# Kernel tuning notes

Measured on AMD Instinct MI355X. Metric: run time of the kernel, lower is better.

The kernel has to match this reference:

```python
import jax, jax.numpy as jnp
import numpy as np

D = 256       # vec_dim
HEADS = 8     # head_num
PS = 4        # patch_size
WS = 7        # window_size (in patches)
P = WS * WS   # tokens per window


def _relative_index():
    # replicates the torch meshgrid / relative coord logic (indexing='ij')
    coords = np.stack(np.meshgrid(np.arange(WS), np.arange(WS), indexing='ij'))  # [2,WS,WS]
    cf = coords.reshape(2, -1)                                                   # [2,P]
    rc = (cf[:, :, None] - cf[:, None, :]).transpose(1, 2, 0)                    # [P,P,2]
    rc[:, :, 0] += WS - 1
    rc[:, :, 1] += WS - 1
    rc[:, :, 1] *= 2 * WS - 1
    return rc.sum(-1)  # [P,P] ints in [0,(2WS-1)^2)


def _shift_mask(ch, cw):
    # standard swin shift mask built on the patch grid (ch, cw)
    fm = np.zeros((ch, cw))
    idx = (slice(0, -WS), slice(-WS, -(WS // 2)), slice(-(WS // 2), None))
    cnt = 0
    for y in idx:
        for x in idx:
            fm[y, x] = cnt
            cnt += 1
    nh, nw = ch // WS, cw // WS
    fm = fm.reshape(nh, WS, nw, WS).transpose(0, 2, 1, 3).reshape(nh * nw, P)
    m = fm[:, None, :] - fm[:, :, None]
    return np.where(m != 0, -100.0, 0.0).astype(np.float32)


def setup_inputs() -> dict:
    key = jax.random.key(0)
    ks = jax.random.split(key, 10)
    N, PN = 8, 3136
    s = 0.02
    return {
        'inputs': jax.random.normal(ks[0], (N, D, PN), jnp.float32),
        'Wk': jax.random.normal(ks[1], (HEADS * D, D), jnp.float32) * s,
        'bk': jax.random.normal(ks[2], (HEADS * D,), jnp.float32) * s,
        'Wq': jax.random.normal(ks[3], (HEADS * D, D), jnp.float32) * s,
        'bq': jax.random.normal(ks[4], (HEADS * D,), jnp.float32) * s,
        'Wv': jax.random.normal(ks[5], (HEADS * D, D), jnp.float32) * s,
        'bv': jax.random.normal(ks[6], (HEADS * D,), jnp.float32) * s,
        'Wo': jax.random.normal(ks[7], (D, HEADS * D), jnp.float32) * s,
        'bo': jax.random.normal(ks[8], (D,), jnp.float32) * s,
        'rel_code': jax.random.normal(ks[9], ((2 * WS - 1) ** 2, HEADS), jnp.float32) * 0.02,
        'h': 224,
        'w': 224,
    }


def _forward(inputs, Wk, bk, Wq, bq, Wv, bv, Wo, bo, rel_code, h, w):
    ch, cw = h // PS, w // PS            # patch grid
    N, _, PN = inputs.shape
    C = D // (PS * PS)
    nh, nw = ch // WS, cw // WS
    WIN = nh * nw

    # patches2features -> pixel-space roll by WS//2 -> features2patches
    x = inputs.reshape(N, C, PS, PS, ch, cw)
    x = x.transpose(0, 1, 4, 2, 5, 3).reshape(N, C, ch * PS, cw * PS)
    x = jnp.roll(x, (WS // 2, WS // 2), axis=(-2, -1))
    x = x.reshape(N, C, ch, PS, cw, PS).transpose(0, 2, 4, 1, 3, 5).reshape(N, PN, D)
    x = x.transpose(0, 2, 1)  # [N,D,PN]

    def proj(W, b):
        e = jnp.einsum('od,ndp->nop', W, x) + b[None, :, None]  # [N,HEADS*D,PN]
        e = e.reshape(N, HEADS, D, ch, cw)
        # window partition: n h d (nh w1)(nw w2) -> n h (nh nw) d (w1 w2)
        e = e.reshape(N, HEADS, D, nh, WS, nw, WS)
        return e.transpose(0, 1, 3, 5, 2, 4, 6).reshape(N, HEADS, WIN, D, P)

    k = proj(Wk, bk)
    q = proj(Wq, bq)
    v = proj(Wv, bv)

    # attn[p,q] = k_p . q_q  (softmax over keys p, axis=3)
    attn = jnp.einsum('nhgdp,nhgdq->nhgpq', k, q) / (D ** 0.5)
    mask = jnp.asarray(_shift_mask(ch, cw))
    attn = attn + mask[None, None]
    rel_idx = _relative_index().ravel()
    rel = rel_code[rel_idx].reshape(P, P, HEADS).transpose(2, 0, 1)  # [H,P,P]
    attn = attn + rel[None, :, None]
    wmap = jax.nn.softmax(attn, axis=3)

    out = jnp.einsum('nhgdp,nhgpq->nhgdq', v, wmap)
    # window merge back to [N,H,D,PN]
    out = out.reshape(N, HEADS, nh, nw, D, WS, WS)
    out = out.transpose(0, 1, 4, 2, 5, 3, 6).reshape(N, HEADS * D, PN)
    return jnp.einsum('od,ndp->nop', Wo, out) + bo[None, :, None]  # [N,D,PN]


def reference(inputs, Wk, bk, Wq, bq, Wv, bv, Wo, bo, rel_code, h, w):
    return _forward(inputs, Wk, bk, Wq, bq, Wv, bv, Wo, bo, rel_code, h, w)
```

## Files before the change

### kernel.cpp

```cpp
#include <hip/hip_runtime.h>
#include <hip/hip_bf16.h>


#define NBATCH 8
#define MSTR   2176
#define TROWS  3200

typedef unsigned short ushort_t;
typedef __attribute__((ext_vector_type(8))) short bf16x8;
typedef __attribute__((ext_vector_type(8))) unsigned short u16x8;
typedef __attribute__((ext_vector_type(4))) float f32x4;

__device__ __forceinline__ float b2f(ushort_t u) {
  union { unsigned int i; float f; } v; v.i = ((unsigned int)u) << 16; return v.f;
}
__device__ __forceinline__ ushort_t f2b(float f) {
  union { float f; unsigned int u; } v; v.f = f;
  unsigned int u = v.u;
  return (ushort_t)((u + 0x7FFFu + ((u >> 16) & 1u)) >> 16);
}
__device__ __forceinline__ int regof(int y) { return (y < 49) ? 0 : ((y < 53) ? 1 : 2); }
__device__ __forceinline__ int div7(int t) { return (t * 37) >> 8; }
__device__ __forceinline__ int tmap(int p, int gi, int gj) {
  int wi = div7(p); return (gi * 7 + wi) * 56 + gj * 7 + (p - wi * 7);
}
__device__ __forceinline__ ushort4 pack4(f32x4 a) {
  ushort4 u; u.x = f2b(a[0]); u.y = f2b(a[1]); u.z = f2b(a[2]); u.w = f2b(a[3]);
  return u;
}
__device__ __forceinline__ void gload_lds16(const ushort_t* g, ushort_t* l) {
  __builtin_amdgcn_global_load_lds(
      (const __attribute__((address_space(1))) void*)g,
      (__attribute__((address_space(3))) void*)l, 16, 0, 0);
}

__global__ void k_prep(const float* __restrict__ Wk, const float* __restrict__ Wq,
                       const float* __restrict__ Wo, const float* __restrict__ Wv,
                       const float* __restrict__ bk, const float* __restrict__ bq,
                       const float* __restrict__ bv, const float* __restrict__ bo,
                       const float* __restrict__ relc,
                       ushort_t* __restrict__ Aext, ushort_t* __restrict__ Wov3,
                       float* __restrict__ cvec, float* __restrict__ relL2) {
  __shared__ float red[8];
  int blk = blockIdx.x, t = threadIdx.x;
  if (blk < 512) {
    int h = blk >> 6, b0 = (blk & 63) << 2, a = t;
    const float* wkh = Wk + h * 65536;
    const float* wqh = Wq + h * 65536;
    float a0 = 0.f, a1 = 0.f, a2 = 0.f, a3 = 0.f;
    for (int dd = 0; dd < 256; ++dd) {
      float wk = wkh[dd * 256 + a];
      float4 w4 = *(const float4*)(wqh + dd * 256 + b0);
      a0 += wk * w4.x; a1 += wk * w4.y; a2 += wk * w4.z; a3 += wk * w4.w;
    }
    ushort4 u; u.x = f2b(a0); u.y = f2b(a1); u.z = f2b(a2); u.w = f2b(a3);
    *(ushort4*)(Aext + (h * 256 + a) * 256 + b0) = u;
  } else if (blk < 1024) {
    int bb = blk - 512;
    int h = bb >> 6, o0 = (bb & 63) << 2, d = t;
    float a0 = 0.f, a1 = 0.f, a2 = 0.f, a3 = 0.f;
    for (int dd = 0; dd < 256; ++dd) {
      float wv = Wv[(h * 256 + dd) * 256 + d];
      a0 += Wo[(o0 + 0) * 2048 + h * 256 + dd] * wv;
      a1 += Wo[(o0 + 1) * 2048 + h * 256 + dd] * wv;
      a2 += Wo[(o0 + 2) * 2048 + h * 256 + dd] * wv;
      a3 += Wo[(o0 + 3) * 2048 + h * 256 + dd] * wv;
    }
    Wov3[(o0 + 0) * 2048 + h * 256 + d] = f2b(a0);
    Wov3[(o0 + 1) * 2048 + h * 256 + d] = f2b(a1);
    Wov3[(o0 + 2) * 2048 + h * 256 + d] = f2b(a2);
    Wov3[(o0 + 3) * 2048 + h * 256 + d] = f2b(a3);
  } else if (blk < 1032) {
    int h = blk - 1024;
    float s1 = 0.f, s2 = 0.f;
    for (int dd = 0; dd < 256; ++dd) {
      s1 += bk[h * 256 + dd] * Wq[(h * 256 + dd) * 256 + t];
      s2 += bq[h * 256 + dd] * Wk[(h * 256 + dd) * 256 + t];
    }
    Aext[(2048 + h) * 256 + t] = f2b(s1);
    Aext[(2056 + h) * 256 + t] = f2b(s2);
  } else if (blk == 1032) {
    for (int i = t; i < 112 * 256 / 8; i += 256)
      *(u16x8*)(Aext + 2064 * 256 + i * 8) = (u16x8){0,0,0,0,0,0,0,0};
  } else if (blk < 1289) {
    int o = blk - 1033;
    const float* wob = Wo + o * 2048;
    float acc = 0.f;
#pragma unroll
    for (int j = 0; j < 8; ++j) acc += wob[j * 256 + t] * bv[j * 256 + t];
#pragma unroll
    for (int s = 1; s < 64; s <<= 1) acc += __shfl_xor(acc, s);
    if ((t & 63) == 0) red[t >> 6] = acc;
    __syncthreads();
    if (t == 0) cvec[o] = bo[o] + red[0] + red[1] + red[2] + red[3];
  } else {
    if (t < 8) {
      float c = 0.f;
      for (int dd = 0; dd < 256; ++dd) c += bk[t * 256 + dd] * bq[t * 256 + dd];
      red[t] = c * 0.0625f;
    }
    __syncthreads();
    for (int i = t; i < 8 * 169; i += 256) {
      int h = i / 169, idx = i - h * 169;
      relL2[i] = relc[idx * 8 + h] + red[h];
    }
  }
}

__global__ void k_conv(const float* __restrict__ X, ushort_t* __restrict__ Xroll) {
  const int n = blockIdx.x / 57, y = blockIdx.x % 57;
  ushort_t* xr = Xroll + (size_t)n * TROWS * 256;
  const int d = threadIdx.x;
  if (y == 56) {
    for (int i = d; i < 64 * 256 / 8; i += 256)
      *(u16x8*)(xr + 3136 * 256 + i * 8) = (u16x8){0,0,0,0,0,0,0,0};
    return;
  }
  const int c = d >> 4, p1 = (d >> 2) & 3, p2 = d & 3;
  const int sp = c * 16 + (((p1 + 1) & 3) << 2) + ((p2 + 1) & 3);
  const int ty = (p1 == 3) ? y : ((y == 0) ? 55 : y - 1);
  const float* rowp = X + (size_t)n * 256 * 3136 + sp * 3136 + ty * 56;
  ushort_t* orow = xr + y * 56 * 256 + d;
  for (int x = 0; x < 56; ++x) {
    int tx = (p2 == 3) ? x : ((x == 0) ? 55 : x - 1);
    orow[x * 256] = f2b(rowp[tx]);
  }
}

__global__ __launch_bounds__(256, 2) void k_gemm1(
    const ushort_t* __restrict__ Xroll, const ushort_t* __restrict__ Aext,
    ushort_t* __restrict__ MT) {
  __shared__ ushort_t Bsm[128 * 256];
  const int bx = blockIdx.x;
  const int n = bx / 425, r = bx % 425;
  const int tt = r / 17, aa = r % 17;
  const int a0 = aa * 128, t0 = tt * 128;
  const int tid = threadIdx.x, wave = tid >> 6, lane = tid & 63;
  const int quad = lane >> 4, l16 = lane & 15;
  const int wa = wave >> 1, wt = wave & 1;
  const ushort_t* Xn = Xroll + (size_t)n * TROWS * 256;
  ushort_t* Mn = MT + (size_t)n * TROWS * MSTR;

#pragma unroll
  for (int i = 0; i < 16; ++i) {
    int S = i * 256 + tid;
    int rr = S >> 5, sc = S & 31;
    int c = (sc & 24) | ((sc ^ rr) & 7);
    gload_lds16(Xn + (t0 + rr) * 256 + c * 8, &Bsm[(i * 256 + wave * 64) * 8]);
  }
  __syncthreads();

  f32x4 acc[4][4];
#pragma unroll
  for (int i = 0; i < 4; ++i)
#pragma unroll
    for (int j = 0; j < 4; ++j) acc[i][j] = (f32x4){0.f, 0.f, 0.f, 0.f};

  const ushort_t* abase = Aext + (a0 + wa * 64 + l16) * 256 + quad * 8;
  const int sw = l16 & 7;
  bf16x8 af[4], afn[4];
#pragma unroll
  for (int i = 0; i < 4; ++i) af[i] = *(const bf16x8*)(abase + i * 4096);
#pragma unroll
  for (int kk = 0; kk < 8; ++kk) {
    if (kk < 7) {
#pragma unroll
      for (int i = 0; i < 4; ++i)
        afn[i] = *(const bf16x8*)(abase + i * 4096 + (kk + 1) * 32);
    }
    bf16x8 bf[4];
#pragma unroll
    for (int j = 0; j < 4; ++j) {
      int rr = wt * 64 + j * 16 + l16;
      int c = kk * 4 + quad;
      int pos = (c & 24) | ((c ^ sw) & 7);
      bf[j] = *(const bf16x8*)(&Bsm[rr * 256 + pos * 8]);
    }
#pragma unroll
    for (int i = 0; i < 4; ++i)
#pragma unroll
      for (int j = 0; j < 4; ++j)
        acc[i][j] = __builtin_amdgcn_mfma_f32_16x16x32_bf16(af[i], bf[j], acc[i][j], 0, 0, 0);
    if (kk < 7) {
#pragma unroll
      for (int i = 0; i < 4; ++i) af[i] = afn[i];
    }
  }
#pragma unroll
  for (int i = 0; i < 4; ++i)
#pragma unroll
    for (int j = 0; j < 4; ++j) {
      int tg = t0 + wt * 64 + j * 16 + l16;
      int ag = a0 + wa * 64 + i * 16 + quad * 4;
      *(ushort4*)(Mn + (size_t)tg * MSTR + ag) = pack4(acc[i][j]);
    }
}

#define XP_STR 264
__global__ __launch_bounds__(512, 4) void k_attn2(
    const ushort_t* __restrict__ Xroll, ushort_t* __restrict__ MT,
    const float* __restrict__ relL2) {
  __shared__ ushort_t Xp[64 * XP_STR];
  __shared__ ushort_t StB[2][64 * 72];
  __shared__ float aqsL[8 * 64];
  __shared__ float bpsL[8 * 64];
  __shared__ float relLh[8 * 169];

  const int tid = threadIdx.x;
  const int wave = tid >> 6, lane = tid & 63;
  const int quad = lane >> 4, l16 = lane & 15;
  const int group = wave >> 2, wv = wave & 3;
  const int n = blockIdx.x >> 6, g = blockIdx.x & 63;
  const int gi = g >> 3, gj = g & 7;
  const ushort_t* Xn = Xroll + (size_t)n * TROWS * 256;
  ushort_t* Mn = MT + (size_t)n * TROWS * MSTR;

  {
    const int p = tid & 63, cg = tid >> 6;
    if (p < 49) {
      int t = tmap(p, gi, gj);
#pragma unroll
      for (int i = 0; i < 4; ++i)
        *(u16x8*)(&Xp[p * XP_STR + (cg * 4 + i) * 8]) =
            *(const u16x8*)(Xn + t * 256 + (cg * 4 + i) * 8);
    } else {
#pragma unroll
      for (int i = 0; i < 4; ++i)
        *(u16x8*)(&Xp[p * XP_STR + (cg * 4 + i) * 8]) = (u16x8){0,0,0,0,0,0,0,0};
    }
  }
  for (int i = tid; i < 8 * 169; i += 512) relLh[i] = relL2[i];
  {
    const int h = tid >> 6, q = tid & 63;
    int qq = (q < 49) ? q : 48;
    int t = tmap(qq, gi, gj);
    aqsL[h * 64 + q] = b2f(Mn[(size_t)t * MSTR + 2048 + h]);
    bpsL[h * 64 + q] = b2f(Mn[(size_t)t * MSTR + 2056 + h]);
  }
  __syncthreads();

  bf16x8 xfr[4][2];
#pragma unroll
  for (int dt = 0; dt < 4; ++dt) {
    const int d = (wv * 4 + dt) * 16 + l16;
#pragma unroll
    for (int kk = 0; kk < 2; ++kk)
#pragma unroll
      for (int j = 0; j < 8; ++j)
        xfr[dt][kk][j] = (short)Xp[(kk * 32 + quad * 8 + j) * XP_STR + d];
  }

  const int q = wv * 16 + l16;
  const int qq = (q < 49) ? q : 48;
  const int tq = tmap(qq, gi, gj);
  const ushort_t* Mbase = Mn + (size_t)tq * MSTR + quad * 8;
  const int yq = div7(qq), xq = qq - yq * 7;
  const int fq = regof(gi * 7 + yq) * 3 + regof(gj * 7 + xq);

  for (int hh = 0; hh < 4; ++hh) {
    const int h = hh * 2 + group;
    f32x4 sacc[4];
#pragma unroll
    for (int pt = 0; pt < 4; ++pt) sacc[pt] = (f32x4){0.f, 0.f, 0.f, 0.f};
    const ushort_t* mrow = Mbase + h * 256;
#pragma unroll
    for (int kk = 0; kk < 8; ++kk) {
      bf16x8 bfm = *(const bf16x8*)(mrow + kk * 32);
#pragma unroll
      for (int pt = 0; pt < 4; ++pt) {
        bf16x8 af = *(const bf16x8*)(&Xp[(pt * 16 + l16) * XP_STR + kk * 32 + quad * 8]);
        sacc[pt] = __builtin_amdgcn_mfma_f32_16x16x32_bf16(af, bfm, sacc[pt], 0, 0, 0);
      }
    }
    float v[16];
    const float aqv = aqsL[h * 64 + q];
    const float* rel_h = &relLh[h * 169];
    float m = -1e30f;
#pragma unroll
    for (int pt = 0; pt < 4; ++pt)
#pragma unroll
      for (int r = 0; r < 4; ++r) {
        int p = pt * 16 + quad * 4 + r;
        float val = -1e30f;
        if (p < 49) {
          int yp = div7(p), xp = p - yp * 7;
          int fp = regof(gi * 7 + yp) * 3 + regof(gj * 7 + xp);
          val = (sacc[pt][r] + aqv + bpsL[h * 64 + p]) * 0.0625f +
                rel_h[(yp - yq + 6) + 13 * (xp - xq + 6)];
          if (fp != fq) val -= 100.f;
        }
        v[pt * 4 + r] = val;
        m = fmaxf(m, val);
      }
    m = fmaxf(m, __shfl_xor(m, 16));
    m = fmaxf(m, __shfl_xor(m, 32));
    float s = 0.f;
#pragma unroll
    for (int i = 0; i < 16; ++i) { v[i] = __expf(v[i] - m); s += v[i]; }
    s += __shfl_xor(s, 16);
    s += __shfl_xor(s, 32);
    const float inv = 1.f / s;
    __syncthreads();
    {
      ushort_t* sb = &StB[group][q * 72];
#pragma unroll
      for (int pt = 0; pt < 4; ++pt) {
        ushort4 u;
        u.x = f2b(v[pt * 4 + 0] * inv); u.y = f2b(v[pt * 4 + 1] * inv);
        u.z = f2b(v[pt * 4 + 2] * inv); u.w = f2b(v[pt * 4 + 3] * inv);
        *(ushort4*)(&sb[pt * 16 + quad * 4]) = u;
      }
    }
    __syncthreads();
#pragma unroll
    for (int qt = 0; qt < 4; ++qt) {
      f32x4 tacc[4];
#pragma unroll
      for (int dt = 0; dt < 4; ++dt) tacc[dt] = (f32x4){0.f, 0.f, 0.f, 0.f};
#pragma unroll
      for (int kk = 0; kk < 2; ++kk) {
        bf16x8 bfw = *(const bf16x8*)(&StB[group][(qt * 16 + l16) * 72 + kk * 32 + quad * 8]);
#pragma unroll
        for (int dt = 0; dt < 4; ++dt)
          tacc[dt] = __builtin_amdgcn_mfma_f32_16x16x32_bf16(xfr[dt][kk], bfw, tacc[dt], 0, 0, 0);
      }
      int q2 = qt * 16 + l16;
      if (q2 < 49) {
        int t2 = tmap(q2, gi, gj);
#pragma unroll
        for (int dt = 0; dt < 4; ++dt) {
          int d0 = (wv * 4 + dt) * 16 + quad * 4;
          *(ushort4*)(Mn + (size_t)t2 * MSTR + h * 256 + d0) = pack4(tacc[dt]);
        }
      }
    }
  }
}

__global__ __launch_bounds__(256, 2) void k_gemm3(
    const ushort_t* __restrict__ Wov3, const ushort_t* __restrict__ MT,
    const float* __restrict__ cvec, float* __restrict__ out) {
  __shared__ ushort_t Asm[128 * 128];
  __shared__ ushort_t Bsm[128 * 128];
  const int bx = blockIdx.x;
  const int n = bx / 50, r2 = bx % 50;
  const int oi = r2 / 25, tt = r2 % 25;
  const int o0 = oi * 128, t0 = tt * 128;
  const int tid = threadIdx.x, wave = tid >> 6, lane = tid & 63;
  const int quad = lane >> 4, l16 = lane & 15;
  const int wa = wave >> 1, wt = wave & 1;
  const ushort_t* Tn = MT + (size_t)n * TROWS * MSTR;
  float* on = out + (size_t)n * 256 * 3136;
  const int sw = l16 & 7;

  f32x4 acc[4][4];
#pragma unroll
  for (int i = 0; i < 4; ++i)
#pragma unroll
    for (int j = 0; j < 4; ++j) acc[i][j] = (f32x4){0.f, 0.f, 0.f, 0.f};

  for (int kit = 0; kit < 16; ++kit) {
    const int kb = kit * 128;
#pragma unroll
    for (int i = 0; i < 8; ++i) {
      int S = i * 256 + tid;
      int rr = S >> 4, sc = S & 15;
      int c = (sc & 8) | ((sc ^ rr) & 7);
      gload_lds16(Wov3 + (o0 + rr) * 2048 + kb + c * 8,
                  &Asm[(i * 256 + wave * 64) * 8]);
    }
#pragma unroll
    for (int i = 0; i < 8; ++i) {
      int S = i * 256 + tid;
      int rr = S >> 4, sc = S & 15;
      int c = (sc & 8) | ((sc ^ rr) & 7);
      gload_lds16(Tn + (size_t)(t0 + rr) * MSTR + kb + c * 8,
                  &Bsm[(i * 256 + wave * 64) * 8]);
    }
    __syncthreads();
#pragma unroll
    for (int kk = 0; kk < 4; ++kk) {
      bf16x8 af[4], bf[4];
      const int c = kk * 4 + quad;
      const int pos = (c & 8) | ((c ^ sw) & 7);
#pragma unroll
      for (int i = 0; i < 4; ++i)
        af[i] = *(const bf16x8*)(&Asm[(wa * 64 + i * 16 + l16) * 128 + pos * 8]);
#pragma unroll
      for (int j = 0; j < 4; ++j)
        bf[j] = *(const bf16x8*)(&Bsm[(wt * 64 + j * 16 + l16) * 128 + pos * 8]);
#pragma unroll
      for (int i = 0; i < 4; ++i)
#pragma unroll
        for (int j = 0; j < 4; ++j)
          acc[i][j] = __builtin_amdgcn_mfma_f32_16x16x32_bf16(af[i], bf[j], acc[i][j], 0, 0, 0);
    }
    __syncthreads();
  }
#pragma unroll
  for (int i = 0; i < 4; ++i) {
    const int ob = o0 + wa * 64 + i * 16 + quad * 4;
    const float4 cv = *(const float4*)(cvec + ob);
#pragma unroll
    for (int j = 0; j < 4; ++j) {
      const int tg = t0 + wt * 64 + j * 16 + l16;
      if (tg < 3136) {
        on[(size_t)(ob + 0) * 3136 + tg] = acc[i][j][0] + cv.x;
        on[(size_t)(ob + 1) * 3136 + tg] = acc[i][j][1] + cv.y;
        on[(size_t)(ob + 2) * 3136 + tg] = acc[i][j][2] + cv.z;
        on[(size_t)(ob + 3) * 3136 + tg] = acc[i][j][3] + cv.w;
      }
    }
  }
}

extern "C" void kernel_launch(void* const* d_in, const int* in_sizes, int n_in,
                              void* d_out, int out_size, void* d_ws, size_t ws_size,
                              hipStream_t stream) {
  (void)in_sizes; (void)n_in; (void)out_size; (void)ws_size;
  const float* X  = (const float*)d_in[0];
  const float* Wk = (const float*)d_in[1];
  const float* bk = (const float*)d_in[2];
  const float* Wq = (const float*)d_in[3];
  const float* bq = (const float*)d_in[4];
  const float* Wv = (const float*)d_in[5];
  const float* bv = (const float*)d_in[6];
  const float* Wo = (const float*)d_in[7];
  const float* bo = (const float*)d_in[8];
  const float* rc = (const float*)d_in[9];

  ushort_t* MT    = (ushort_t*)d_ws;
  ushort_t* Xroll = MT + (size_t)8 * TROWS * MSTR;
  ushort_t* Aext  = Xroll + (size_t)8 * TROWS * 256;
  ushort_t* Wov3  = Aext + 2176 * 256;
  float* fbase = (float*)(Wov3 + 256 * 2048);
  float* cvec  = fbase;
  float* relL2 = fbase + 256;
  float* out = (float*)d_out;

  k_prep <<<dim3(1290), dim3(256), 0, stream>>>(Wk, Wq, Wo, Wv, bk, bq, bv, bo, rc,
                                                Aext, Wov3, cvec, relL2);
  k_conv <<<dim3(8 * 57), dim3(256), 0, stream>>>(X, Xroll);
  k_gemm1<<<dim3(8 * 425), dim3(256), 0, stream>>>(Xroll, Aext, MT);
  k_attn2<<<dim3(8 * 64), dim3(512), 0, stream>>>(Xroll, MT, relL2);
  k_gemm3<<<dim3(8 * 50), dim3(256), 0, stream>>>(Wov3, MT, cvec, out);
}
```

Before: 324.0 us.

## Make gemm1 persistent over token tiles with register-resident A and double-buffered LDS

k_gemm1 now launches 8*136 blocks. Each block keeps its 128-row slice of Aext in registers for the full K=256 and loops over 6–7 token tiles of 64 rows. The next token tiles are prefetched into a double-buffered LDS via global_load_lds, with explicit vmcnt waits and barriers. This removes repeated A reloads per tile and overlaps global loads with MFMA compute. The batch index becomes the fastest-varying block index, and k_gemm3 gets a matching block remap, presumably to improve L2/XCD locality. The risks are higher register pressure from holding 16 bf16x8 A fragments and fewer blocks in flight.

Result: faster. 278.2 us (-14.1%).

```diff
diff --git a/kernel.cpp b/kernel.cpp
--- a/kernel.cpp
+++ b/kernel.cpp
@@ -33,6 +33,7 @@
       (const __attribute__((address_space(1))) void*)g,
       (__attribute__((address_space(3))) void*)l, 16, 0, 0);
 }
+__device__ __forceinline__ void sb0() { __builtin_amdgcn_sched_barrier(0); }
 
 __global__ void k_prep(const float* __restrict__ Wk, const float* __restrict__ Wq,
                        const float* __restrict__ Wo, const float* __restrict__ Wv,
@@ -130,70 +131,88 @@
 __global__ __launch_bounds__(256, 2) void k_gemm1(
     const ushort_t* __restrict__ Xroll, const ushort_t* __restrict__ Aext,
     ushort_t* __restrict__ MT) {
-  __shared__ ushort_t Bsm[128 * 256];
-  const int bx = blockIdx.x;
-  const int n = bx / 425, r = bx % 425;
-  const int tt = r / 17, aa = r % 17;
-  const int a0 = aa * 128, t0 = tt * 128;
+  __shared__ ushort_t Bsm[2][64 * 256];
+  const int bx0 = blockIdx.x;
+  const int n = bx0 & 7;
+  const int inner = bx0 >> 3;
+  const int aa = inner % 17;
+  const int c  = inner / 17;
+  const int a0 = aa * 128;
+  const int tstart = c * 6 + ((c < 2) ? c : 2);
+  const int T = 6 + ((c < 2) ? 1 : 0);
   const int tid = threadIdx.x, wave = tid >> 6, lane = tid & 63;
   const int quad = lane >> 4, l16 = lane & 15;
-  const int wa = wave >> 1, wt = wave & 1;
   const ushort_t* Xn = Xroll + (size_t)n * TROWS * 256;
   ushort_t* Mn = MT + (size_t)n * TROWS * MSTR;
 
-#pragma unroll
-  for (int i = 0; i < 16; ++i) {
-    int S = i * 256 + tid;
-    int rr = S >> 5, sc = S & 31;
-    int c = (sc & 24) | ((sc ^ rr) & 7);
-    gload_lds16(Xn + (t0 + rr) * 256 + c * 8, &Bsm[(i * 256 + wave * 64) * 8]);
-  }
-  __syncthreads();
-
-  f32x4 acc[4][4];
-#pragma unroll
-  for (int i = 0; i < 4; ++i)
-#pragma unroll
-    for (int j = 0; j < 4; ++j) acc[i][j] = (f32x4){0.f, 0.f, 0.f, 0.f};
-
-  const ushort_t* abase = Aext + (a0 + wa * 64 + l16) * 256 + quad * 8;
+  const ushort_t* abase = Aext + (size_t)(a0 + wave * 32 + l16) * 256 + quad * 8;
+  bf16x8 areg[8][2];
+#pragma unroll
+  for (int kk = 0; kk < 8; ++kk)
+#pragma unroll
+    for (int i = 0; i < 2; ++i)
+      areg[kk][i] = *(const bf16x8*)(abase + i * 4096 + kk * 32);
+  sb0();
+
+  auto fill = [&](int mt, int b) {
+    const ushort_t* src = Xn + (size_t)(tstart + mt) * 64 * 256;
+#pragma unroll
+    for (int i = 0; i < 8; ++i) {
+      int S = i * 256 + tid;
+      int rr = S >> 5, sc = S & 31;
+      int cc = (sc & 24) | ((sc ^ rr) & 7);
+      gload_lds16(src + rr * 256 + cc * 8, &Bsm[b][(i * 256 + wave * 64) * 8]);
+    }
+  };
+
+  fill(0, 0); sb0();
+  fill(1, 1); sb0();
+  asm volatile("s_waitcnt vmcnt(8)" ::: "memory"); sb0();
+  __builtin_amdgcn_s_barrier(); sb0();
+
   const int sw = l16 & 7;
-  bf16x8 af[4], afn[4];
-#pragma unroll
-  for (int i = 0; i < 4; ++i) af[i] = *(const bf16x8*)(abase + i * 4096);
-#pragma unroll
-  for (int kk = 0; kk < 8; ++kk) {
-    if (kk < 7) {
-#pragma unroll
-      for (int i = 0; i < 4; ++i)
-        afn[i] = *(const bf16x8*)(abase + i * 4096 + (kk + 1) * 32);
-    }
-    bf16x8 bf[4];
-#pragma unroll
-    for (int j = 0; j < 4; ++j) {
-      int rr = wt * 64 + j * 16 + l16;
-      int c = kk * 4 + quad;
-      int pos = (c & 24) | ((c ^ sw) & 7);
-      bf[j] = *(const bf16x8*)(&Bsm[rr * 256 + pos * 8]);
-    }
-#pragma unroll
-    for (int i = 0; i < 4; ++i)
-#pragma unroll
-      for (int j = 0; j < 4; ++j)
-        acc[i][j] = __builtin_amdgcn_mfma_f32_16x16x32_bf16(af[i], bf[j], acc[i][j], 0, 0, 0);
-    if (kk < 7) {
-#pragma unroll
-      for (int i = 0; i < 4; ++i) af[i] = afn[i];
-    }
-  }
-#pragma unroll
-  for (int i = 0; i < 4; ++i)
-#pragma unroll
-    for (int j = 0; j < 4; ++j) {
-      int tg = t0 + wt * 64 + j * 16 + l16;
-      int ag = a0 + wa * 64 + i * 16 + quad * 4;
-      *(ushort4*)(Mn + (size_t)tg * MSTR + ag) = pack4(acc[i][j]);
-    }
+  for (int m = 0; m < T; ++m) {
+    if (m > 0) {
+      if (m + 1 < T) { asm volatile("s_waitcnt vmcnt(16)" ::: "memory"); }
+      else           { asm volatile("s_waitcnt vmcnt(8)"  ::: "memory"); }
+      sb0();
+      __builtin_amdgcn_s_barrier(); sb0();
+    }
+    const int b = m & 1;
+    f32x4 acc[2][4];
+#pragma unroll
+    for (int i = 0; i < 2; ++i)
+#pragma unroll
+      for (int j = 0; j < 4; ++j) acc[i][j] = (f32x4){0.f, 0.f, 0.f, 0.f};
+#pragma unroll
+    for (int kk = 0; kk < 8; ++kk) {
+      bf16x8 bfj[4];
+#pragma unroll
+      for (int j = 0; j < 4; ++j) {
+        int rr = j * 16 + l16;
+        int cc = kk * 4 + quad;
+        int pos = (cc & 24) | ((cc ^ sw) & 7);
+        bfj[j] = *(const bf16x8*)(&Bsm[b][rr * 256 + pos * 8]);
+      }
+#pragma unroll
+      for (int i = 0; i < 2; ++i)
+#pragma unroll
+        for (int j = 0; j < 4; ++j)
+          acc[i][j] = __builtin_amdgcn_mfma_f32_16x16x32_bf16(areg[kk][i], bfj[j], acc[i][j], 0, 0, 0);
+    }
+    const int tb = (tstart + m) * 64;
+#pragma unroll
+    for (int i = 0; i < 2; ++i)
+#pragma unroll
+      for (int j = 0; j < 4; ++j) {
+        int tg = tb + j * 16 + l16;
+        int ag = a0 + wave * 32 + i * 16 + quad * 4;
+        *(ushort4*)(Mn + (size_t)tg * MSTR + ag) = pack4(acc[i][j]);
+      }
+    sb0();
+    __builtin_amdgcn_s_barrier(); sb0();
+    if (m + 2 < T) { fill(m + 2, b); sb0(); }
+  }
 }
 
 #define XP_STR 264
@@ -342,7 +361,8 @@
     const float* __restrict__ cvec, float* __restrict__ out) {
   __shared__ ushort_t Asm[128 * 128];
   __shared__ ushort_t Bsm[128 * 128];
-  const int bx = blockIdx.x;
+  const int bx0 = blockIdx.x;
+  const int bx = (bx0 & 7) * 50 + (bx0 >> 3);
   const int n = bx / 50, r2 = bx % 50;
   const int oi = r2 / 25, tt = r2 % 25;
   const int o0 = oi * 128, t0 = tt * 128;
@@ -441,7 +461,7 @@
   k_prep <<<dim3(1290), dim3(256), 0, stream>>>(Wk, Wq, Wo, Wv, bk, bq, bv, bo, rc,
                                                 Aext, Wov3, cvec, relL2);
   k_conv <<<dim3(8 * 57), dim3(256), 0, stream>>>(X, Xroll);
-  k_gemm1<<<dim3(8 * 425), dim3(256), 0, stream>>>(Xroll, Aext, MT);
+  k_gemm1<<<dim3(8 * 136), dim3(256), 0, stream>>>(Xroll, Aext, MT);
   k_attn2<<<dim3(8 * 64), dim3(512), 0, stream>>>(Xroll, MT, relL2);
   k_gemm3<<<dim3(8 * 50), dim3(256), 0, stream>>>(Wov3, MT, cvec, out);
 }
```
